# Kernel tuning notes

Hardware: AMD Instinct MI355X
Metric: run time of the kernel (lower is better)

The kernel has to match this reference:

```python
import jax, jax.numpy as jnp
import numpy as np

CUBE = (80, 80, 20)
NBINS = CUBE[0] * CUBE[1] * CUBE[2]  # 128000
NVIEW = 5
B = 2
C_IMG, C_FEAT = 3, 32
H_IMG, W_IMG = 512, 512
H_F, W_F = 128, 128
HID = 256
IN_DIM = 3 + 2 * (C_IMG + C_FEAT)  # 73


def setup_inputs() -> dict:
    key = jax.random.key(0)
    ks = jax.random.split(key, 8)
    denorm_imgs = jax.random.uniform(ks[0], (NVIEW, B, C_IMG, H_IMG, W_IMG), jnp.float32)
    feats2d = jax.random.normal(ks[1], (NVIEW, B, C_FEAT, H_F, W_F), jnp.float32)
    # grid_sample coords in [-1, 1], last dim = (x, y)
    sample_grid = jax.random.uniform(ks[2], (NVIEW, NBINS, 2), jnp.float32, -1.0, 1.0)
    points = jax.random.normal(ks[3], (NBINS, 3), jnp.float32)
    W1 = jax.random.normal(ks[4], (IN_DIM, HID), jnp.float32) * (1.0 / np.sqrt(IN_DIM))
    b1 = jnp.zeros((HID,), jnp.float32)
    W2 = jax.random.normal(ks[5], (HID, 1), jnp.float32) * (1.0 / np.sqrt(HID))
    b2 = jnp.zeros((1,), jnp.float32)
    return {"denorm_imgs": denorm_imgs, "feats2d": feats2d, "sample_grid": sample_grid,
            "points": points, "W1": W1, "b1": b1, "W2": W2, "b2": b2}


def _grid_sample(img, grid):
    """Bilinear grid_sample, align_corners=True, padding_mode='zeros'.
    img: [B, C, H, W]; grid: [N, 2] in [-1, 1] (x, y). Returns [B, C, N]."""
    H, W = img.shape[-2], img.shape[-1]
    ix = (grid[:, 0] + 1.0) * 0.5 * (W - 1)
    iy = (grid[:, 1] + 1.0) * 0.5 * (H - 1)
    x0 = jnp.floor(ix)
    y0 = jnp.floor(iy)
    x1 = x0 + 1.0
    y1 = y0 + 1.0
    wx1 = ix - x0
    wx0 = 1.0 - wx1
    wy1 = iy - y0
    wy0 = 1.0 - wy1

    def corner(x, y, w):
        valid = ((x >= 0) & (x <= W - 1) & (y >= 0) & (y <= H - 1)).astype(img.dtype)
        xi = jnp.clip(x, 0, W - 1).astype(jnp.int32)
        yi = jnp.clip(y, 0, H - 1).astype(jnp.int32)
        vals = img[:, :, yi, xi]  # [B, C, N]
        return vals * (w * valid)[None, None, :]

    return (corner(x0, y0, wx0 * wy0) + corner(x1, y0, wx1 * wy0)
            + corner(x0, y1, wx0 * wy1) + corner(x1, y1, wx1 * wy1))


def reference(denorm_imgs, feats2d, sample_grid, points, W1, b1, W2, b2):
    # Batched multi-view grid_sample: [V, B, C, N]
    cubes_img = jax.vmap(_grid_sample)(denorm_imgs, sample_grid)
    cubes_feat = jax.vmap(_grid_sample)(feats2d, sample_grid)
    cubes = jnp.concatenate([cubes_img, cubes_feat], axis=2)  # [V, B, C_tot, N]
    cubes = jnp.transpose(cubes, (1, 2, 3, 0))  # [B, C_tot, N, V]
    nview = cubes.shape[-1]
    mean = jnp.sum(cubes, axis=-1, keepdims=True) / nview          # [B, C, N, 1]
    var = jnp.sum((cubes - mean) ** 2, axis=-1, keepdims=True) / nview
    var = jnp.exp(-var)
    gvol = jnp.concatenate([mean[..., 0], var[..., 0]], axis=1)    # [B, 2C, N]
    feats = jnp.transpose(gvol, (0, 2, 1))                         # [B, N, 2C]
    bsz = feats.shape[0]
    pts = jnp.broadcast_to(points[None], (bsz,) + points.shape)    # [B, N, 3]
    inp = jnp.concatenate([pts, feats], axis=-1)                   # [B, N, 3+2C]
    h = jax.nn.relu(inp @ W1 + b1)
    density = jax.nn.softplus(h @ W2 + b2)                         # [B, N, 1]
    alpha = 1.0 - jnp.exp(-density)
    return alpha.reshape(bsz, 1, CUBE[0], CUBE[1], CUBE[2])
```

## Files before the change

kernel.cpp:

```cpp
#include <hip/hip_runtime.h>

#define NVIEW 5
#define NB    128000
#define CF    32
#define HID   256
#define KA    96
#define IMG_HW 262144
#define FT_HW  16384

typedef __attribute__((ext_vector_type(8))) short short8;
typedef __attribute__((ext_vector_type(4))) float f32x4;

__device__ __forceinline__ unsigned int f2bf(float f) {
    unsigned int u = __float_as_uint(f);
    return (u + 0x7fffu + ((u >> 16) & 1u)) >> 16;
}
__device__ __forceinline__ unsigned int pk(float a, float b) {
    return f2bf(a) | (f2bf(b) << 16);
}
__device__ __forceinline__ float b2f_lo(unsigned int u) { return __uint_as_float(u << 16); }
__device__ __forceinline__ float b2f_hi(unsigned int u) { return __uint_as_float(u & 0xffff0000u); }

__device__ __forceinline__ int mapk(int k) {
    if (k < 22) return k;
    if (k < 25) return k + 16;
    if (k == 25) return -1;
    if (k < 42) return k + 15;
    if (k < 48) return -1;
    if (k < 64) return k - 26;
    if (k < 80) return k - 7;
    return -1;
}

__global__ __launch_bounds__(256) void prep(
    const float* __restrict__ imgs, const float* __restrict__ feats,
    const float* __restrict__ W1, const float* __restrict__ b1,
    const float* __restrict__ W2, const float* __restrict__ b2,
    uint4* __restrict__ imgsP, uint4* __restrict__ featsP,
    unsigned int* __restrict__ Bfrag, float* __restrict__ bw)
{
    const int bidx = blockIdx.x;
    const int t = threadIdx.x;
    if (bidx < 5120) {
        int gid = bidx * 256 + t;
        int v  = gid >> 18;
        int px = gid & (IMG_HW - 1);
        const float* base = imgs + (size_t)v * 6 * IMG_HW + px;
        uint4 o;
        o.x = f2bf(base[0 * IMG_HW]) | (f2bf(base[1 * IMG_HW]) << 16);
        o.y = f2bf(base[2 * IMG_HW]);
        o.z = f2bf(base[3 * IMG_HW]) | (f2bf(base[4 * IMG_HW]) << 16);
        o.w = f2bf(base[5 * IMG_HW]);
        imgsP[gid] = o;
    } else if (bidx < 6400) {
        __shared__ unsigned short tile[64][65];
        const int pixbase = (bidx - 5120) * 64;
        const int v   = pixbase >> 14;
        const int rem = pixbase & 16383;
        {
            const int p = t & 63;
            const int s = t >> 6;
            #pragma unroll
            for (int it = 0; it < 16; it++) {
                int plane = it * 4 + s;
                tile[plane][p] =
                    (unsigned short)f2bf(feats[((size_t)v * 64 + plane) * FT_HW + rem + p]);
            }
        }
        __syncthreads();
        {
            const int q = t & 7;
            #pragma unroll
            for (int it = 0; it < 2; it++) {
                int p = it * 32 + (t >> 3);
                uint4 o;
                o.x = (unsigned)tile[q * 8 + 0][p] | ((unsigned)tile[q * 8 + 1][p] << 16);
                o.y = (unsigned)tile[q * 8 + 2][p] | ((unsigned)tile[q * 8 + 3][p] << 16);
                o.z = (unsigned)tile[q * 8 + 4][p] | ((unsigned)tile[q * 8 + 5][p] << 16);
                o.w = (unsigned)tile[q * 8 + 6][p] | ((unsigned)tile[q * 8 + 7][p] << 16);
                featsP[(size_t)(pixbase + p) * 8 + q] = o;
            }
        }
    } else {
        int e = (bidx - 6400) * 256 + t;
        int ju = e & 3;
        int nn = (e >> 2) & 255;
        int o  = e >> 10;
        int k0 = o * 8 + ju * 2;
        int i0 = mapk(k0), i1 = mapk(k0 + 1);
        float f0 = (i0 >= 0) ? W1[i0 * 256 + nn] : 0.f;
        float f1 = (i1 >= 0) ? W1[i1 * 256 + nn] : 0.f;
        Bfrag[e] = pk(f0, f1);
        if (e < 256)       bw[e] = b1[e];
        else if (e < 512)  bw[e] = W2[e - 256];
        else if (e == 512) bw[e] = b2[0];
    }
}

#define AROW 13

__global__ __launch_bounds__(256, 2) void fused_gather_mlp(
    const unsigned short* __restrict__ imgsP,
    const unsigned short* __restrict__ featsP,
    const float* __restrict__ grid,
    const float* __restrict__ points,
    const unsigned int*   __restrict__ Bfrag,
    const float*          __restrict__ bw,
    float* __restrict__ out)
{
    __shared__ unsigned int Bl[12288];
    __shared__ uint4 As4[128 * AROW];
    __shared__ float b1s[HID];
    __shared__ float W2s[HID];

    const int tid = threadIdx.x;

    {
        const uint4* src = (const uint4*)Bfrag;
        uint4* dst = (uint4*)Bl;
        #pragma unroll
        for (int i = 0; i < 12; i++) dst[i * 256 + tid] = src[i * 256 + tid];
        b1s[tid] = bw[tid];
        W2s[tid] = bw[256 + tid];
    }
    const float b2v = bw[512];

    const int n    = blockIdx.x * 64 + (tid >> 2);
    const int b    = (tid >> 1) & 1;
    const int half = tid & 1;

    float sumf[16], ssqf[16];
    #pragma unroll
    for (int c = 0; c < 16; c++) { sumf[c] = 0.f; ssqf[c] = 0.f; }
    float si0 = 0.f, si1 = 0.f, si2 = 0.f;
    float qi0 = 0.f, qi1 = 0.f, qi2 = 0.f;
    float p0 = 0.f, p1 = 0.f, p2 = 0.f;
    if (half == 0) {
        p0 = points[n * 3 + 0];
        p1 = points[n * 3 + 1];
        p2 = points[n * 3 + 2];
    }

    #pragma unroll
    for (int v = 0; v < NVIEW; v++) {
        const float2 g = ((const float2*)grid)[v * NB + n];
        const float gx = g.x, gy = g.y;

        if (half == 0) {
            float ix = (gx + 1.f) * 0.5f * 511.f;
            float iy = (gy + 1.f) * 0.5f * 511.f;
            float x0f = floorf(ix), y0f = floorf(iy);
            float x1f = x0f + 1.f, y1f = y0f + 1.f;
            float wx1 = ix - x0f, wx0 = 1.f - wx1;
            float wy1 = iy - y0f, wy0 = 1.f - wy1;
            float vi0 = 0.f, vi1 = 0.f, vi2 = 0.f;
            const unsigned short* base = imgsP + ((size_t)v * IMG_HW) * 8 + b * 4;
            #pragma unroll
            for (int k = 0; k < 4; k++) {
                float xf = (k & 1) ? x1f : x0f;
                float yf = (k >> 1) ? y1f : y0f;
                float w  = ((k & 1) ? wx1 : wx0) * ((k >> 1) ? wy1 : wy0);
                float vd = (xf >= 0.f && xf <= 511.f && yf >= 0.f && yf <= 511.f) ? 1.f : 0.f;
                w *= vd;
                int xi = (int)fminf(fmaxf(xf, 0.f), 511.f);
                int yi = (int)fminf(fmaxf(yf, 0.f), 511.f);
                uint2 iv = *(const uint2*)(base + (size_t)(yi * 512 + xi) * 8);
                vi0 += w * b2f_lo(iv.x);
                vi1 += w * b2f_hi(iv.x);
                vi2 += w * b2f_lo(iv.y);
            }
            si0 += vi0; qi0 += vi0 * vi0;
            si1 += vi1; qi1 += vi1 * vi1;
            si2 += vi2; qi2 += vi2 * vi2;
        }

        {
            float ix = (gx + 1.f) * 0.5f * 127.f;
            float iy = (gy + 1.f) * 0.5f * 127.f;
            float x0f = floorf(ix), y0f = floorf(iy);
            float x1f = x0f + 1.f, y1f = y0f + 1.f;
            float wx1 = ix - x0f, wx0 = 1.f - wx1;
            float wy1 = iy - y0f, wy0 = 1.f - wy1;
            const unsigned short* fb =
                featsP + ((size_t)v * FT_HW) * 64 + b * 32 + half * 16;
            float val[16];
            #pragma unroll
            for (int c = 0; c < 16; c++) val[c] = 0.f;
            #pragma unroll
            for (int k = 0; k < 4; k++) {
                float xf = (k & 1) ? x1f : x0f;
                float yf = (k >> 1) ? y1f : y0f;
                float w  = ((k & 1) ? wx1 : wx0) * ((k >> 1) ? wy1 : wy0);
                float vd = (xf >= 0.f && xf <= 127.f && yf >= 0.f && yf <= 127.f) ? 1.f : 0.f;
                w *= vd;
                int xi = (int)fminf(fmaxf(xf, 0.f), 127.f);
                int yi = (int)fminf(fmaxf(yf, 0.f), 127.f);
                const uint4* p = (const uint4*)(fb + (size_t)(yi * 128 + xi) * 64);
                #pragma unroll
                for (int q = 0; q < 2; q++) {
                    uint4 f4 = p[q];
                    val[q * 8 + 0] += w * b2f_lo(f4.x);
                    val[q * 8 + 1] += w * b2f_hi(f4.x);
                    val[q * 8 + 2] += w * b2f_lo(f4.y);
                    val[q * 8 + 3] += w * b2f_hi(f4.y);
                    val[q * 8 + 4] += w * b2f_lo(f4.z);
                    val[q * 8 + 5] += w * b2f_hi(f4.z);
                    val[q * 8 + 6] += w * b2f_lo(f4.w);
                    val[q * 8 + 7] += w * b2f_hi(f4.w);
                }
            }
            #pragma unroll
            for (int c = 0; c < 16; c++) {
                sumf[c] += val[c];
                ssqf[c] += val[c] * val[c];
            }
        }
    }

    #pragma unroll
    for (int c = 0; c < 16; c++) {
        float m = sumf[c] * 0.2f;
        float q = ssqf[c] * 0.2f - m * m;
        sumf[c] = m;
        ssqf[c] = expf(-q);
    }
    float mi0 = si0 * 0.2f, mi1 = si1 * 0.2f, mi2 = si2 * 0.2f;
    float ei0 = expf(-(qi0 * 0.2f - mi0 * mi0));
    float ei1 = expf(-(qi1 * 0.2f - mi1 * mi1));
    float ei2 = expf(-(qi2 * 0.2f - mi2 * mi2));

    unsigned int u[24];
    if (half == 0) {
        u[0] = pk(p0, p1);
        u[1] = pk(p2, mi0);
        u[2] = pk(mi1, mi2);
        #pragma unroll
        for (int j = 0; j < 8; j++) u[3 + j] = pk(sumf[2 * j], sumf[2 * j + 1]);
        u[11] = pk(ei0, ei1);
        u[12] = pk(ei2, 0.f);
        #pragma unroll
        for (int j = 0; j < 8; j++) u[13 + j] = pk(ssqf[2 * j], ssqf[2 * j + 1]);
        u[21] = 0u; u[22] = 0u; u[23] = 0u;
    } else {
        #pragma unroll
        for (int j = 0; j < 8; j++) u[j]     = pk(sumf[2 * j], sumf[2 * j + 1]);
        #pragma unroll
        for (int j = 0; j < 8; j++) u[8 + j] = pk(ssqf[2 * j], ssqf[2 * j + 1]);
        #pragma unroll
        for (int j = 16; j < 24; j++) u[j] = 0u;
    }

    {
        uint4* arow = &As4[(tid >> 1) * AROW + half * 6];
        #pragma unroll
        for (int i = 0; i < 6; i++)
            arow[i] = make_uint4(u[4 * i], u[4 * i + 1], u[4 * i + 2], u[4 * i + 3]);
    }
    __syncthreads();

    const int w    = tid >> 6;
    const int lane = tid & 63;
    const int col  = lane & 15;
    const int quad = lane >> 4;
    const long rowbase = (long)blockIdx.x * 128 + w * 32;

    f32x4 acc[2][16];
    #pragma unroll
    for (int m = 0; m < 2; m++)
        #pragma unroll
        for (int t = 0; t < 16; t++)
            acc[m][t] = (f32x4){0.f, 0.f, 0.f, 0.f};

    const unsigned int* bp = Bl + (quad * 256 + col) * 4;

    #pragma unroll
    for (int s = 0; s < 3; s++) {
        short8 af0 = *(const short8*)&As4[(w * 32 + col)      * AROW + s * 4 + quad];
        short8 af1 = *(const short8*)&As4[(w * 32 + 16 + col) * AROW + s * 4 + quad];
        #pragma unroll
        for (int t = 0; t < 16; t++) {
            short8 bf = *(const short8*)(bp + s * 4096 + t * 64);
            acc[0][t] = __builtin_amdgcn_mfma_f32_16x16x32_bf16(af0, bf, acc[0][t], 0, 0, 0);
            acc[1][t] = __builtin_amdgcn_mfma_f32_16x16x32_bf16(af1, bf, acc[1][t], 0, 0, 0);
        }
    }

    float pm[2][4] = {{0.f, 0.f, 0.f, 0.f}, {0.f, 0.f, 0.f, 0.f}};
    #pragma unroll
    for (int t = 0; t < 16; t++) {
        float b1v = b1s[t * 16 + col];
        float w2v = W2s[t * 16 + col];
        #pragma unroll
        for (int m = 0; m < 2; m++)
            #pragma unroll
            for (int r = 0; r < 4; r++) {
                float h = fmaxf(acc[m][t][r] + b1v, 0.f);
                pm[m][r] += h * w2v;
            }
    }
    #pragma unroll
    for (int m = 0; m < 2; m++)
        #pragma unroll
        for (int r = 0; r < 4; r++) {
            float p = pm[m][r];
            p += __shfl_xor(p, 1);
            p += __shfl_xor(p, 2);
            p += __shfl_xor(p, 4);
            p += __shfl_xor(p, 8);
            pm[m][r] = p;
        }

    if (col == 0) {
        #pragma unroll
        for (int m = 0; m < 2; m++)
            #pragma unroll
            for (int r = 0; r < 4; r++) {
                float x  = pm[m][r] + b2v;
                float sp = fmaxf(x, 0.f) + log1pf(expf(-fabsf(x)));
                float alpha = -expm1f(-sp);
                long row = rowbase + m * 16 + quad * 4 + r;
                out[(row & 1) * (long)NB + (row >> 1)] = alpha;
            }
    }
}

extern "C" void kernel_launch(void* const* d_in, const int* in_sizes, int n_in,
                              void* d_out, int out_size, void* d_ws, size_t ws_size,
                              hipStream_t stream) {
    const float* imgs   = (const float*)d_in[0];
    const float* feats  = (const float*)d_in[1];
    const float* grid   = (const float*)d_in[2];
    const float* points = (const float*)d_in[3];
    const float* W1     = (const float*)d_in[4];
    const float* b1     = (const float*)d_in[5];
    const float* W2     = (const float*)d_in[6];
    const float* b2     = (const float*)d_in[7];
    float* out = (float*)d_out;

    unsigned short* imgsP  = (unsigned short*)d_ws;
    unsigned short* featsP = imgsP + (size_t)NVIEW * IMG_HW * 8;
    unsigned int*   Bfrag  = (unsigned int*)(featsP + (size_t)NVIEW * FT_HW * 64);
    float*          bwbuf  = (float*)(Bfrag + 12288);

    prep<<<dim3(6448), dim3(256), 0, stream>>>(
        imgs, feats, W1, b1, W2, b2,
        (uint4*)imgsP, (uint4*)featsP, Bfrag, bwbuf);
    fused_gather_mlp<<<dim3(2000), dim3(256), 0, stream>>>(
        imgsP, featsP, grid, points, Bfrag, bwbuf, out);
}
```

Measured before the change: 194.5 us.

## Drop LDS weight staging, split MLP into halves, vectorize image prep

The image-packing part of prep now has each thread handle four pixels with float4 loads, which cuts the block count. The main kernel no longer copies the 48KB W1 fragment into LDS; B fragments are read straight from global memory (L2/L1 cached), and the hidden dimension is processed in two halves of eight tiles, so half as many accumulators are live. Launch bounds rise to 3 blocks per SM to raise occupancy. The trade is more global or cache traffic for weights per MFMA in exchange for less LDS, fewer registers and no block-start copy.

```diff
diff --git a/kernel.cpp b/kernel.cpp
--- a/kernel.cpp
+++ b/kernel.cpp
@@ -41,20 +41,29 @@
 {
     const int bidx = blockIdx.x;
     const int t = threadIdx.x;
-    if (bidx < 5120) {
+    if (bidx < 1280) {
         int gid = bidx * 256 + t;
-        int v  = gid >> 18;
-        int px = gid & (IMG_HW - 1);
+        int v   = gid >> 16;
+        int px  = (gid & 65535) * 4;
         const float* base = imgs + (size_t)v * 6 * IMG_HW + px;
-        uint4 o;
-        o.x = f2bf(base[0 * IMG_HW]) | (f2bf(base[1 * IMG_HW]) << 16);
-        o.y = f2bf(base[2 * IMG_HW]);
-        o.z = f2bf(base[3 * IMG_HW]) | (f2bf(base[4 * IMG_HW]) << 16);
-        o.w = f2bf(base[5 * IMG_HW]);
-        imgsP[gid] = o;
-    } else if (bidx < 6400) {
+        float4 pl[6];
+        #pragma unroll
+        for (int p = 0; p < 6; p++)
+            pl[p] = *(const float4*)(base + (size_t)p * IMG_HW);
+        uint4 o[4];
+        #pragma unroll
+        for (int i = 0; i < 4; i++) {
+            float c0 = ((const float*)&pl[0])[i], c1 = ((const float*)&pl[1])[i];
+            float c2 = ((const float*)&pl[2])[i], c3 = ((const float*)&pl[3])[i];
+            float c4 = ((const float*)&pl[4])[i], c5 = ((const float*)&pl[5])[i];
+            o[i] = make_uint4(pk(c0, c1), f2bf(c2), pk(c3, c4), f2bf(c5));
+        }
+        #pragma unroll
+        for (int i = 0; i < 4; i++)
+            imgsP[(size_t)v * IMG_HW + px + i] = o[i];
+    } else if (bidx < 2560) {
         __shared__ unsigned short tile[64][65];
-        const int pixbase = (bidx - 5120) * 64;
+        const int pixbase = (bidx - 1280) * 64;
         const int v   = pixbase >> 14;
         const int rem = pixbase & 16383;
         {
@@ -82,7 +91,7 @@
             }
         }
     } else {
-        int e = (bidx - 6400) * 256 + t;
+        int e = (bidx - 2560) * 256 + t;
         int ju = e & 3;
         int nn = (e >> 2) & 255;
         int o  = e >> 10;
@@ -99,7 +108,7 @@
 
 #define AROW 13
 
-__global__ __launch_bounds__(256, 2) void fused_gather_mlp(
+__global__ __launch_bounds__(256, 3) void fused_gather_mlp(
     const unsigned short* __restrict__ imgsP,
     const unsigned short* __restrict__ featsP,
     const float* __restrict__ grid,
@@ -108,21 +117,13 @@
     const float*          __restrict__ bw,
     float* __restrict__ out)
 {
-    __shared__ unsigned int Bl[12288];
     __shared__ uint4 As4[128 * AROW];
     __shared__ float b1s[HID];
     __shared__ float W2s[HID];
 
     const int tid = threadIdx.x;
-
-    {
-        const uint4* src = (const uint4*)Bfrag;
-        uint4* dst = (uint4*)Bl;
-        #pragma unroll
-        for (int i = 0; i < 12; i++) dst[i * 256 + tid] = src[i * 256 + tid];
-        b1s[tid] = bw[tid];
-        W2s[tid] = bw[256 + tid];
-    }
+    b1s[tid] = bw[tid];
+    W2s[tid] = bw[256 + tid];
     const float b2v = bw[512];
 
     const int n    = blockIdx.x * 64 + (tid >> 2);
@@ -264,40 +265,50 @@
     const int quad = lane >> 4;
     const long rowbase = (long)blockIdx.x * 128 + w * 32;
 
-    f32x4 acc[2][16];
-    #pragma unroll
-    for (int m = 0; m < 2; m++)
-        #pragma unroll
-        for (int t = 0; t < 16; t++)
-            acc[m][t] = (f32x4){0.f, 0.f, 0.f, 0.f};
-
-    const unsigned int* bp = Bl + (quad * 256 + col) * 4;
-
+    short8 af[2][3];
     #pragma unroll
     for (int s = 0; s < 3; s++) {
-        short8 af0 = *(const short8*)&As4[(w * 32 + col)      * AROW + s * 4 + quad];
-        short8 af1 = *(const short8*)&As4[(w * 32 + 16 + col) * AROW + s * 4 + quad];
-        #pragma unroll
-        for (int t = 0; t < 16; t++) {
-            short8 bf = *(const short8*)(bp + s * 4096 + t * 64);
-            acc[0][t] = __builtin_amdgcn_mfma_f32_16x16x32_bf16(af0, bf, acc[0][t], 0, 0, 0);
-            acc[1][t] = __builtin_amdgcn_mfma_f32_16x16x32_bf16(af1, bf, acc[1][t], 0, 0, 0);
-        }
-    }
+        af[0][s] = *(const short8*)&As4[(w * 32 + col)      * AROW + s * 4 + quad];
+        af[1][s] = *(const short8*)&As4[(w * 32 + 16 + col) * AROW + s * 4 + quad];
+    }
+
+    const unsigned int* bpg = Bfrag + (quad * 256 + col) * 4;
 
     float pm[2][4] = {{0.f, 0.f, 0.f, 0.f}, {0.f, 0.f, 0.f, 0.f}};
     #pragma unroll
-    for (int t = 0; t < 16; t++) {
-        float b1v = b1s[t * 16 + col];
-        float w2v = W2s[t * 16 + col];
+    for (int h = 0; h < 2; h++) {
+        f32x4 acc[2][8];
         #pragma unroll
         for (int m = 0; m < 2; m++)
             #pragma unroll
-            for (int r = 0; r < 4; r++) {
-                float h = fmaxf(acc[m][t][r] + b1v, 0.f);
-                pm[m][r] += h * w2v;
-            }
-    }
+            for (int t = 0; t < 8; t++)
+                acc[m][t] = (f32x4){0.f, 0.f, 0.f, 0.f};
+
+        #pragma unroll
+        for (int s = 0; s < 3; s++) {
+            #pragma unroll
+            for (int t = 0; t < 8; t++) {
+                short8 bf = *(const short8*)(bpg + s * 4096 + (h * 8 + t) * 64);
+                acc[0][t] = __builtin_amdgcn_mfma_f32_16x16x32_bf16(af[0][s], bf, acc[0][t], 0, 0, 0);
+                acc[1][t] = __builtin_amdgcn_mfma_f32_16x16x32_bf16(af[1][s], bf, acc[1][t], 0, 0, 0);
+            }
+        }
+
+        #pragma unroll
+        for (int t = 0; t < 8; t++) {
+            int j = h * 128 + t * 16 + col;
+            float b1v = b1s[j];
+            float w2v = W2s[j];
+            #pragma unroll
+            for (int m = 0; m < 2; m++)
+                #pragma unroll
+                for (int r = 0; r < 4; r++) {
+                    float hh = fmaxf(acc[m][t][r] + b1v, 0.f);
+                    pm[m][r] += hh * w2v;
+                }
+        }
+    }
+
     #pragma unroll
     for (int m = 0; m < 2; m++)
         #pragma unroll
@@ -342,7 +353,7 @@
     unsigned int*   Bfrag  = (unsigned int*)(featsP + (size_t)NVIEW * FT_HW * 64);
     float*          bwbuf  = (float*)(Bfrag + 12288);
 
-    prep<<<dim3(6448), dim3(256), 0, stream>>>(
+    prep<<<dim3(2608), dim3(256), 0, stream>>>(
         imgs, feats, W1, b1, W2, b2,
         (uint4*)imgsP, (uint4*)featsP, Bfrag, bwbuf);
     fused_gather_mlp<<<dim3(2000), dim3(256), 0, stream>>>(
```

Result: slower. 208.9 us (+7.4%).
